# Kernel tuning notes

Measured on AMD Instinct MI355X. Metric: run time of the kernel, lower is better.

The kernel has to match this reference:

```python
import jax, jax.numpy as jnp
import numpy as np

N, D, H, E, TOP_K = 32768, 768, 256, 8, 2


def setup_inputs() -> dict:
    key = jax.random.key(0)
    ks = jax.random.split(key, 9)
    s_in = 1.0 / np.sqrt(D)
    s_hid = 1.0 / np.sqrt(H)
    return {
        "x": jax.random.normal(ks[0], (N, D), dtype=jnp.float32),
        # per-expert MLP weights, stacked over expert dim E
        "W1": jax.random.uniform(ks[1], (E, D, H), jnp.float32, -s_in, s_in),
        "b1": jax.random.uniform(ks[2], (E, H), jnp.float32, -s_in, s_in),
        "W2": jax.random.uniform(ks[3], (E, H, D), jnp.float32, -s_hid, s_hid),
        "b2": jax.random.uniform(ks[4], (E, D), jnp.float32, -s_hid, s_hid),
        # gate MLP: Linear(D,H) -> ReLU -> Linear(H,E)
        "Wg1": jax.random.uniform(ks[5], (D, H), jnp.float32, -s_in, s_in),
        "bg1": jax.random.uniform(ks[6], (H,), jnp.float32, -s_in, s_in),
        "Wg2": jax.random.uniform(ks[7], (H, E), jnp.float32, -s_hid, s_hid),
        "bg2": jax.random.uniform(ks[8], (E,), jnp.float32, -s_hid, s_hid),
    }


def reference(x, W1, b1, W2, b2, Wg1, bg1, Wg2, bg2):
    # gating
    gate_scores = jax.nn.relu(x @ Wg1 + bg1) @ Wg2 + bg2          # [N, E]
    gate_probs = jax.nn.softmax(gate_scores, axis=-1)              # [N, E]
    top_k_probs, top_k_idx = jax.lax.top_k(gate_probs, TOP_K)      # [N, K]
    top_k_probs = top_k_probs / jnp.sum(top_k_probs, axis=-1, keepdims=True)

    # dense all-expert compute (faithful to original: every expert on every token)
    h = jax.nn.relu(jnp.einsum("nd,edh->enh", x, W1) + b1[:, None, :])  # [E, N, H]
    expert_out = jnp.einsum("enh,ehd->end", h, W2) + b2[:, None, :]      # [E, N, D]

    # gather selected experts per token and combine
    tok = jnp.arange(x.shape[0])[:, None]                          # [N, 1]
    sel = expert_out[top_k_idx, tok, :]                            # [N, K, D]
    output = jnp.sum(top_k_probs[..., None] * sel, axis=1)          # [N, D]
    return output, gate_probs
```

## Files before the change

### kernel.cpp

```cpp
#include <hip/hip_runtime.h>
#include <hip/hip_bf16.h>
#include <stdint.h>

#define NTOK 32768
#define DIM  768
#define HID  256
#define NEXP 8
#define PADC 144

typedef float f32x4 __attribute__((ext_vector_type(4)));
typedef short s16x8 __attribute__((ext_vector_type(8)));

__device__ __forceinline__ unsigned short f2bf(float f) {
  union { float f; unsigned int u; } c; c.f = f;
  unsigned int r = c.u + 0x7fffu + ((c.u >> 16) & 1u);
  return (unsigned short)(r >> 16);
}

__device__ __forceinline__ float bf2f(unsigned int u) {
  union { unsigned int x; float f; } c; c.x = u << 16; return c.f;
}

__device__ __forceinline__ unsigned short f2h(float f) {
  union { _Float16 h; unsigned short u; } c; c.h = (_Float16)f; return c.u;
}

__device__ __forceinline__ float h2f(unsigned short u) {
  union { unsigned short u; _Float16 h; } c; c.u = u; return (float)c.h;
}

__device__ __forceinline__ void gload_lds16(const unsigned short* g, unsigned short* l) {
  __builtin_amdgcn_global_load_lds((const __attribute__((address_space(1))) void*)g,
                                   (__attribute__((address_space(3))) void*)l, 16, 0, 0);
}

__global__ __launch_bounds__(256) void k_cvt_x(const float* __restrict__ x,
                                               unsigned short* __restrict__ xf16) {
  int i = (blockIdx.x * 256 + threadIdx.x) * 8;
  float4 a = *(const float4*)(x + i);
  float4 b = *(const float4*)(x + i + 4);
  float f[8] = {a.x, a.y, a.z, a.w, b.x, b.y, b.z, b.w};
  unsigned short hh[8];
#pragma unroll
  for (int q = 0; q < 8; ++q) hh[q] = f2h(f[q]);
  int4 vh;
  vh.x = (int)((unsigned)hh[0] | ((unsigned)hh[1] << 16));
  vh.y = (int)((unsigned)hh[2] | ((unsigned)hh[3] << 16));
  vh.z = (int)((unsigned)hh[4] | ((unsigned)hh[5] << 16));
  vh.w = (int)((unsigned)hh[6] | ((unsigned)hh[7] << 16));
  *(int4*)(xf16 + i) = vh;
}

__global__ __launch_bounds__(256) void k_trall(const float* __restrict__ W1,
                                               const float* __restrict__ Wg1,
                                               const float* __restrict__ W2,
                                               unsigned short* __restrict__ w1t,
                                               unsigned short* __restrict__ wg1t,
                                               unsigned short* __restrict__ w2t) {
  __shared__ float tile[32][33];
  int z = blockIdx.z;
  const float* ip;
  unsigned short* op;
  int R, C;
  if (z < 8)       { ip = W1 + (size_t)z * DIM * HID;  op = w1t + (size_t)z * DIM * HID;  R = DIM; C = HID; }
  else if (z == 8) { ip = Wg1;                          op = wg1t;                          R = DIM; C = HID; }
  else             { ip = W2 + (size_t)(z - 9) * HID * DIM; op = w2t + (size_t)(z - 9) * HID * DIM; R = HID; C = DIM; }
  int r0 = blockIdx.y * 32, c0 = blockIdx.x * 32;
  if (r0 >= R || c0 >= C) return;
  int tx = threadIdx.x & 31, ty = threadIdx.x >> 5;
#pragma unroll
  for (int i = 0; i < 4; ++i)
    tile[ty + i * 8][tx] = ip[(size_t)(r0 + ty + i * 8) * C + c0 + tx];
  __syncthreads();
#pragma unroll
  for (int i = 0; i < 4; ++i)
    op[(size_t)(c0 + ty + i * 8) * R + r0 + tx] = f2h(tile[tx][ty + i * 8]);
}

__global__ __launch_bounds__(512) void k_gate1f(const unsigned short* __restrict__ xf16,
                                                const unsigned short* __restrict__ wg1t,
                                                const float* __restrict__ bg1,
                                                const float* __restrict__ wg2,
                                                const float* __restrict__ bg2,
                                                float* __restrict__ gs,
                                                int* __restrict__ rcnt,
                                                int* __restrict__ rlist) {
  int bm = blockIdx.x * 128;

  __shared__ __align__(16) unsigned short smem[(1024 + 2048) * 8];
  unsigned short* hs = smem;
  float* sc = (float*)&smem[16896];
  float* wg2s = (float*)&smem[20480];

  int tid = threadIdx.x;
  int lane = tid & 63;
  int wid = tid >> 6;
  int wm = wid >> 2, wn = wid & 3;
  int ar = lane & 15, kg = lane >> 4;

  const unsigned short* asrc[2];
  unsigned short* ldsA[2];
#pragma unroll
  for (int q = 0; q < 2; ++q) {
    int cb0 = q * 512 + wid * 64;
    int ci = cb0 + lane;
    int row = ci >> 3;
    int cb = (ci & 7) ^ (row & 7);
    asrc[q] = xf16 + (size_t)(bm + row) * DIM + cb * 8;
    ldsA[q] = &smem[cb0 * 8];
  }
  const unsigned short* bsrc[4];
  unsigned short* ldsB[4];
#pragma unroll
  for (int q = 0; q < 4; ++q) {
    int cb0 = q * 512 + wid * 64;
    int ci = cb0 + lane;
    int row = ci >> 3;
    int cb = (ci & 7) ^ (row & 7);
    bsrc[q] = wg1t + (size_t)row * DIM + cb * 8;
    ldsB[q] = &smem[8192 + cb0 * 8];
  }

  f32x4 acc[4][4] = {};

  for (int kt = 0; kt < DIM / 64; ++kt) {
#pragma unroll
    for (int q = 0; q < 2; ++q) gload_lds16(asrc[q] + kt * 64, ldsA[q]);
#pragma unroll
    for (int q = 0; q < 4; ++q) gload_lds16(bsrc[q] + kt * 64, ldsB[q]);
    __syncthreads();
#pragma unroll
    for (int ks = 0; ks < 2; ++ks) {
      int kc = ks * 4 + kg;
      s16x8 a[4], b[4];
#pragma unroll
      for (int m = 0; m < 4; ++m) {
        int row = wm * 64 + m * 16 + ar;
        a[m] = *(const s16x8*)&smem[row * 64 + ((kc ^ (row & 7)) * 8)];
      }
#pragma unroll
      for (int n = 0; n < 4; ++n) {
        int row = wn * 64 + n * 16 + ar;
        b[n] = *(const s16x8*)&smem[8192 + row * 64 + ((kc ^ (row & 7)) * 8)];
      }
#pragma unroll
      for (int m = 0; m < 4; ++m)
#pragma unroll
        for (int n = 0; n < 4; ++n)
          acc[m][n] = __builtin_amdgcn_mfma_f32_16x16x32_f16(a[m], b[n], acc[m][n], 0, 0, 0);
    }
    __syncthreads();
  }

#pragma unroll
  for (int j = 0; j < 4; ++j) wg2s[tid * 4 + j] = wg2[tid * 4 + j];

  int tok2 = (tid & 63) * 2;
  int ex = tid >> 6;
  float s0 = 0.f, s1 = 0.f;
#pragma unroll 1
  for (int half = 0; half < 2; ++half) {
    if ((wn >> 1) == half) {
#pragma unroll
      for (int n = 0; n < 4; ++n) {
        int col = (wn & 1) * 64 + n * 16 + ar;
        float bb = bg1[half * 128 + col];
#pragma unroll
        for (int m = 0; m < 4; ++m) {
          int rbase = wm * 64 + m * 16 + kg * 4;
#pragma unroll
          for (int r = 0; r < 4; ++r)
            hs[col * 132 + rbase + r] = f2h(fmaxf(acc[m][n][r] + bb, 0.f));
        }
      }
    }
    __syncthreads();
#pragma unroll 8
    for (int c = 0; c < 128; ++c) {
      unsigned int pair = *(const unsigned int*)&hs[c * 132 + tok2];
      float h0 = h2f((unsigned short)(pair & 0xffffu));
      float h1 = h2f((unsigned short)(pair >> 16));
      float w = wg2s[(half * 128 + c) * 8 + ex];
      s0 = fmaf(h0, w, s0);
      s1 = fmaf(h1, w, s1);
    }
    __syncthreads();
  }

  float b2e = bg2[ex];
  s0 += b2e; s1 += b2e;
  gs[(size_t)(bm + tok2) * 8 + ex] = s0;
  gs[(size_t)(bm + tok2 + 1) * 8 + ex] = s1;
  sc[tok2 * 8 + ex] = s0;
  sc[tok2 * 8 + 8 + ex] = s1;
  __syncthreads();

  if (tid < 128) {
    float m1 = -3e38f, m2 = -3e38f, m3 = -3e38f;
#pragma unroll
    for (int e = 0; e < 8; ++e) {
      float v = sc[tid * 8 + e];
      if (v > m1)      { m3 = m2; m2 = m1; m1 = v; }
      else if (v > m2) { m3 = m2; m2 = v; }
      else if (v > m3) { m3 = v; }
    }
    if (m2 - m3 < 1e-3f) {
      int i = atomicAdd(rcnt, 1);
      rlist[i] = bm + tid;
    }
  }
}

__global__ __launch_bounds__(256) void k_rescue(const float* __restrict__ x,
                                                const float* __restrict__ wg1,
                                                const float* __restrict__ bg1,
                                                const float* __restrict__ wg2,
                                                const float* __restrict__ bg2,
                                                const int* __restrict__ rcnt,
                                                const int* __restrict__ rlist,
                                                float* __restrict__ gs) {
  __shared__ float xs[DIM];
  __shared__ float ps[4][8];
  int n = rcnt[0];
  int tid = threadIdx.x;
  int lane = tid & 63, wid = tid >> 6;
  for (int idx = blockIdx.x; idx < n; idx += 2048) {
    int tok = rlist[idx];
    __syncthreads();
#pragma unroll
    for (int q = 0; q < 3; ++q) xs[tid + q * 256] = x[(size_t)tok * DIM + tid + q * 256];
    __syncthreads();
    const float* wcol = wg1 + tid;
    float pa[8] = {};
#pragma unroll 4
    for (int k0 = 0; k0 < DIM; k0 += 8) {
#pragma unroll
      for (int q = 0; q < 8; ++q)
        pa[q] = fmaf(xs[k0 + q], wcol[(size_t)(k0 + q) * HID], pa[q]);
    }
    float acc = bg1[tid] +
                (((pa[0] + pa[1]) + (pa[2] + pa[3])) + ((pa[4] + pa[5]) + (pa[6] + pa[7])));
    float hj = fmaxf(acc, 0.f);
    float p[8];
#pragma unroll
    for (int e = 0; e < 8; ++e) p[e] = hj * wg2[tid * 8 + e];
#pragma unroll
    for (int off = 32; off >= 1; off >>= 1) {
#pragma unroll
      for (int e = 0; e < 8; ++e) p[e] += __shfl_xor(p[e], off);
    }
    if (lane == 0) {
#pragma unroll
      for (int e = 0; e < 8; ++e) ps[wid][e] = p[e];
    }
    __syncthreads();
    if (tid < 8)
      gs[(size_t)tok * 8 + tid] = bg2[tid] + ps[0][tid] + ps[1][tid] + ps[2][tid] + ps[3][tid];
  }
}

__global__ __launch_bounds__(256) void k_gate2b(const float* __restrict__ gs,
                                                float* __restrict__ gprob,
                                                int* __restrict__ cnt,
                                                int* __restrict__ lists,
                                                float* __restrict__ wts) {
  __shared__ int lcnt[8];
  __shared__ int sbase[8];
  __shared__ int se1[256], se2[256], sp1[256], sp2[256];
  __shared__ float sw1[256], sw2[256];
  int tid = threadIdx.x;
  if (tid < 8) lcnt[tid] = 0;
  __syncthreads();

  int tok = blockIdx.x * 256 + tid;
  f32x4 s0v = *(const f32x4*)&gs[(size_t)tok * 8];
  f32x4 s1v = *(const f32x4*)&gs[(size_t)tok * 8 + 4];
  float s[8] = {s0v[0], s0v[1], s0v[2], s0v[3], s1v[0], s1v[1], s1v[2], s1v[3]};

  float m = s[0];
#pragma unroll
  for (int e = 1; e < 8; ++e) m = fmaxf(m, s[e]);
  float p[8]; float sum = 0.f;
#pragma unroll
  for (int e = 0; e < 8; ++e) { p[e] = expf(s[e] - m); sum += p[e]; }
  float inv = 1.f / sum;
#pragma unroll
  for (int e = 0; e < 8; ++e) p[e] *= inv;

  f32x4 o0 = {p[0], p[1], p[2], p[3]};
  f32x4 o1 = {p[4], p[5], p[6], p[7]};
  *(f32x4*)&gprob[(size_t)tok * 8] = o0;
  *(f32x4*)&gprob[(size_t)tok * 8 + 4] = o1;

  int e1 = 0; float p1 = p[0];
#pragma unroll
  for (int e = 1; e < 8; ++e) if (p[e] > p1) { p1 = p[e]; e1 = e; }
  int e2 = -1; float p2 = -1.f;
#pragma unroll
  for (int e = 0; e < 8; ++e) if (e != e1 && p[e] > p2) { p2 = p[e]; e2 = e; }
  float rinv = 1.f / (p1 + p2);

  int pos1 = atomicAdd(&lcnt[e1], 1);
  int pos2 = atomicAdd(&lcnt[e2], 1);
  se1[tid] = e1; sp1[tid] = pos1; sw1[tid] = p1 * rinv;
  se2[tid] = e2; sp2[tid] = pos2; sw2[tid] = p2 * rinv;
  __syncthreads();

  if (tid < 8) sbase[tid] = atomicAdd(&cnt[tid * 32], lcnt[tid]);
  __syncthreads();

  int a1i = sbase[se1[tid]] + sp1[tid];
  lists[se1[tid] * NTOK + a1i] = tok; wts[se1[tid] * NTOK + a1i] = sw1[tid];
  int a2i = sbase[se2[tid]] + sp2[tid];
  lists[se2[tid] * NTOK + a2i] = tok; wts[se2[tid] * NTOK + a2i] = -sw2[tid];
}

__global__ __launch_bounds__(512) void k_ffn1(const unsigned short* __restrict__ xf16,
                                              const unsigned short* __restrict__ w1t,
                                              const float* __restrict__ b1,
                                              const int* __restrict__ cnt,
                                              const int* __restrict__ lists,
                                              unsigned short* __restrict__ h) {
  int id = blockIdx.x;
  int xcd = id & 7, local = id >> 3;
  int xh = local & 31, e = local >> 5;
  int row0 = ((xh << 3) | xcd) * 128;

  int c = cnt[e * 32];
  if (row0 >= c) return;
  int pfx = 0;
#pragma unroll
  for (int j = 0; j < 8; ++j) if (j < e) pfx += cnt[j * 32];

  __shared__ __align__(16) unsigned short smem[(1024 + 2048) * 8];
  __shared__ int stok[128];

  int tid = threadIdx.x;
  int lane = tid & 63;
  int wid = tid >> 6;
  int wm = wid >> 2, wn = wid & 3;
  int ar = lane & 15, kg = lane >> 4;

  if (tid < 128) stok[tid] = lists[e * NTOK + min(row0 + tid, c - 1)];
  __syncthreads();

  const unsigned short* asrc[2];
  unsigned short* ldsA[2];
#pragma unroll
  for (int q = 0; q < 2; ++q) {
    int cb0 = q * 512 + wid * 64;
    int ci = cb0 + lane;
    int row = ci >> 3;
    int cb = (ci & 7) ^ (row & 7);
    asrc[q] = xf16 + (size_t)stok[row] * DIM + cb * 8;
    ldsA[q] = &smem[cb0 * 8];
  }
  const unsigned short* bsrc[4];
  unsigned short* ldsB[4];
#pragma unroll
  for (int q = 0; q < 4; ++q) {
    int cb0 = q * 512 + wid * 64;
    int ci = cb0 + lane;
    int row = ci >> 3;
    int cb = (ci & 7) ^ (row & 7);
    bsrc[q] = w1t + ((size_t)e * HID + row) * DIM + cb * 8;
    ldsB[q] = &smem[8192 + cb0 * 8];
  }

  f32x4 acc[4][4] = {};

  for (int kt = 0; kt < DIM / 64; ++kt) {
#pragma unroll
    for (int q = 0; q < 2; ++q) gload_lds16(asrc[q] + kt * 64, ldsA[q]);
#pragma unroll
    for (int q = 0; q < 4; ++q) gload_lds16(bsrc[q] + kt * 64, ldsB[q]);
    __syncthreads();
#pragma unroll
    for (int ks = 0; ks < 2; ++ks) {
      int kc = ks * 4 + kg;
      s16x8 a[4], b[4];
#pragma unroll
      for (int m = 0; m < 4; ++m) {
        int row = wm * 64 + m * 16 + ar;
        a[m] = *(const s16x8*)&smem[row * 64 + ((kc ^ (row & 7)) * 8)];
      }
#pragma unroll
      for (int n = 0; n < 4; ++n) {
        int row = wn * 64 + n * 16 + ar;
        b[n] = *(const s16x8*)&smem[8192 + row * 64 + ((kc ^ (row & 7)) * 8)];
      }
#pragma unroll
      for (int m = 0; m < 4; ++m)
#pragma unroll
        for (int n = 0; n < 4; ++n)
          acc[m][n] = __builtin_amdgcn_mfma_f32_16x16x32_f16(a[m], b[n], acc[m][n], 0, 0, 0);
    }
    __syncthreads();
  }

  int hbase = pfx + row0;
#pragma unroll 1
  for (int half = 0; half < 2; ++half) {
    if ((wn >> 1) == half) {
#pragma unroll
      for (int n = 0; n < 4; ++n) {
        int col = (wn & 1) * 64 + n * 16 + ar;
        float bb = b1[e * HID + half * 128 + col];
#pragma unroll
        for (int m = 0; m < 4; ++m) {
          int rloc = wm * 64 + m * 16 + kg * 4;
#pragma unroll
          for (int r = 0; r < 4; ++r)
            smem[(rloc + r) * PADC + col] = f2h(fmaxf(acc[m][n][r] + bb, 0.f));
        }
      }
    }
    __syncthreads();
#pragma unroll
    for (int q = 0; q < 4; ++q) {
      int ci = tid + q * 512;
      int row = ci >> 4, ch = ci & 15;
      if (row0 + row < c) {
        int4 v = *(const int4*)&smem[row * PADC + ch * 8];
        *(int4*)&h[(size_t)(hbase + row) * HID + half * 128 + ch * 8] = v;
      }
    }
    __syncthreads();
  }
}

template <bool STORE_PART>
__global__ __launch_bounds__(256) void k_ffn2(const unsigned short* __restrict__ h,
                                              const unsigned short* __restrict__ w2t,
                                              const float* __restrict__ b2,
                                              const int* __restrict__ cnt,
                                              const int* __restrict__ lists,
                                              const float* __restrict__ wts,
                                              unsigned short* __restrict__ part0,
                                              unsigned short* __restrict__ part1,
                                              float* __restrict__ out) {
  int id = blockIdx.x;
  int xcd = id & 7, local = id >> 3;
  int bny = local % 6;
  int r2 = local / 6;
  int xh = r2 & 31, e = r2 >> 5;
  int row0 = ((xh << 3) | xcd) * 128;
  int bn = bny * 128;

  int c = cnt[e * 32];
  if (row0 >= c) return;
  int pfx = 0;
#pragma unroll
  for (int j = 0; j < 8; ++j) if (j < e) pfx += cnt[j * 32];

  __shared__ __align__(16) unsigned short smem[128 * PADC];
  __shared__ int stok[128];
  __shared__ float swt[128];
  unsigned short* As = smem;
  unsigned short* Bs = smem + 128 * 64;

  int tid = threadIdx.x;
  int lane = tid & 63;
  int wid = tid >> 6;
  int wm = wid >> 1, wn = wid & 1;
  int ar = lane & 15, kg = lane >> 4;

  if (tid < 128) {
    int r = row0 + tid;
    stok[tid] = (r < c) ? lists[e * NTOK + r] : 0;
    swt[tid]  = (r < c) ? wts[e * NTOK + r] : 0.f;
  }
  __syncthreads();

  const unsigned short* asrc[4];
  const unsigned short* bsrc[4];
  unsigned short* ldsA[4];
  unsigned short* ldsB[4];
#pragma unroll
  for (int i = 0; i < 4; ++i) {
    int cb0 = i * 256 + wid * 64;
    int ci = cb0 + lane;
    int row = ci >> 3;
    int cb = (ci & 7) ^ (row & 7);
    asrc[i] = h + (size_t)(pfx + row0 + row) * HID + cb * 8;
    bsrc[i] = w2t + ((size_t)e * DIM + bn + row) * HID + cb * 8;
    ldsA[i] = &As[cb0 * 8];
    ldsB[i] = &Bs[cb0 * 8];
  }

  f32x4 acc[4][4] = {};

  for (int kt = 0; kt < HID / 64; ++kt) {
#pragma unroll
    for (int i = 0; i < 4; ++i) {
      gload_lds16(asrc[i] + kt * 64, ldsA[i]);
      gload_lds16(bsrc[i] + kt * 64, ldsB[i]);
    }
    __syncthreads();
#pragma unroll
    for (int ks = 0; ks < 2; ++ks) {
      int kc = ks * 4 + kg;
      s16x8 a[4], b[4];
#pragma unroll
      for (int m = 0; m < 4; ++m) {
        int row = wm * 64 + m * 16 + ar;
        a[m] = *(const s16x8*)&As[row * 64 + ((kc ^ (row & 7)) * 8)];
      }
#pragma unroll
      for (int n = 0; n < 4; ++n) {
        int row = wn * 64 + n * 16 + ar;
        b[n] = *(const s16x8*)&Bs[row * 64 + ((kc ^ (row & 7)) * 8)];
      }
#pragma unroll
      for (int m = 0; m < 4; ++m)
#pragma unroll
        for (int n = 0; n < 4; ++n)
          acc[m][n] = __builtin_amdgcn_mfma_f32_16x16x32_f16(a[m], b[n], acc[m][n], 0, 0, 0);
    }
    __syncthreads();
  }

  if constexpr (STORE_PART) {
#pragma unroll
    for (int n = 0; n < 4; ++n) {
      int col = wn * 64 + n * 16 + ar;
      float bb = b2[e * DIM + bn + col];
#pragma unroll
      for (int m = 0; m < 4; ++m) {
        int rloc = wm * 64 + m * 16 + kg * 4;
#pragma unroll
        for (int r = 0; r < 4; ++r) {
          float w = swt[rloc + r];
          smem[(rloc + r) * PADC + col] = f2bf((acc[m][n][r] + bb) * fabsf(w));
        }
      }
    }
    __syncthreads();
#pragma unroll
    for (int q = 0; q < 8; ++q) {
      int ci = tid + q * 256;
      int row = ci >> 4, ch = ci & 15;
      float w = swt[row];
      if (w != 0.f) {
        unsigned short* dst = (w > 0.f) ? part0 : part1;
        int4 v = *(const int4*)&smem[row * PADC + ch * 8];
        *(int4*)&dst[(size_t)stok[row] * DIM + bn + ch * 8] = v;
      }
    }
  } else {
#pragma unroll
    for (int n = 0; n < 4; ++n) {
      int col = bn + wn * 64 + n * 16 + ar;
      float bb = b2[e * DIM + col];
#pragma unroll
      for (int m = 0; m < 4; ++m) {
        int rloc = wm * 64 + m * 16 + kg * 4;
#pragma unroll
        for (int r = 0; r < 4; ++r) {
          float w = swt[rloc + r];
          if (w != 0.f) {
            float v = (acc[m][n][r] + bb) * fabsf(w);
            atomicAdd(&out[(size_t)stok[rloc + r] * DIM + col], v);
          }
        }
      }
    }
  }
}

__global__ __launch_bounds__(256) void k_combine(const unsigned short* __restrict__ p0,
                                                 const unsigned short* __restrict__ p1,
                                                 float* __restrict__ out) {
  size_t i = ((size_t)blockIdx.x * 256 + threadIdx.x) * 8;
  int4 a = *(const int4*)(p0 + i);
  int4 b = *(const int4*)(p1 + i);
  unsigned int ua[4] = {(unsigned)a.x, (unsigned)a.y, (unsigned)a.z, (unsigned)a.w};
  unsigned int ub[4] = {(unsigned)b.x, (unsigned)b.y, (unsigned)b.z, (unsigned)b.w};
  float o[8];
#pragma unroll
  for (int q = 0; q < 4; ++q) {
    o[q * 2 + 0] = bf2f(ua[q] & 0xffffu) + bf2f(ub[q] & 0xffffu);
    o[q * 2 + 1] = bf2f(ua[q] >> 16)     + bf2f(ub[q] >> 16);
  }
  *(float4*)(out + i)     = *(float4*)&o[0];
  *(float4*)(out + i + 4) = *(float4*)&o[4];
}

extern "C" void kernel_launch(void* const* d_in, const int* in_sizes, int n_in,
                              void* d_out, int out_size, void* d_ws, size_t ws_size,
                              hipStream_t stream) {
  const float* x   = (const float*)d_in[0];
  const float* W1  = (const float*)d_in[1];
  const float* b1  = (const float*)d_in[2];
  const float* W2  = (const float*)d_in[3];
  const float* b2  = (const float*)d_in[4];
  const float* Wg1 = (const float*)d_in[5];
  const float* bg1 = (const float*)d_in[6];
  const float* Wg2 = (const float*)d_in[7];
  const float* bg2 = (const float*)d_in[8];
  float* out = (float*)d_out;
  float* gprob = out + (size_t)NTOK * DIM;

  char* ws = (char*)d_ws;
  size_t off = 0;
  auto alloc = [&](size_t bytes) { void* pp = ws + off; off += (bytes + 255) & ~(size_t)255; return pp; };
  unsigned short* w1t = (unsigned short*)alloc((size_t)NEXP * HID * DIM * 2);
  unsigned short* w2t = (unsigned short*)alloc((size_t)NEXP * DIM * HID * 2);
  float* hgbuf = (float*)alloc((size_t)NTOK * HID * 4);
  int* cnt = (int*)alloc(NEXP * 32 * 4 + 256);
  int* lists = (int*)alloc((size_t)NEXP * NTOK * 4);
  float* wts = (float*)alloc((size_t)NEXP * NTOK * 4);
  unsigned short* part0 = (unsigned short*)alloc((size_t)NTOK * DIM * 2);
  unsigned short* part1 = (unsigned short*)alloc((size_t)NTOK * DIM * 2);
  bool store_mode = (off <= ws_size);

  int* rcnt = cnt + NEXP * 32;

  unsigned short *xf16, *wg1t;
  float* gs; int* rlist;
  if (store_mode) {
    xf16 = part1;
    wg1t = part0;
    char* p0b = (char*)part0;
    gs    = (float*)(p0b + (1u << 20));
    rlist = (int*)(p0b + 10 * (1u << 18));
  } else {
    xf16  = (unsigned short*)alloc((size_t)NTOK * DIM * 2);
    wg1t  = (unsigned short*)alloc((size_t)DIM * HID * 2);
    gs    = (float*)alloc((size_t)NTOK * 8 * 4);
    rlist = (int*)alloc((size_t)NTOK * 4);
  }

  unsigned short* h = (unsigned short*)hgbuf;

  hipMemsetAsync(cnt, 0, NEXP * 32 * sizeof(int) + 256, stream);
  if (!store_mode)
    hipMemsetAsync(d_out, 0, (size_t)NTOK * DIM * sizeof(float), stream);

  k_cvt_x<<<(NTOK * DIM) / (256 * 8), 256, 0, stream>>>(x, xf16);
  k_trall<<<dim3(DIM / 32, DIM / 32, 17), 256, 0, stream>>>(W1, Wg1, W2, w1t, wg1t, w2t);
  k_gate1f<<<NTOK / 128, 512, 0, stream>>>(xf16, wg1t, bg1, Wg2, bg2, gs, rcnt, rlist);
  k_rescue<<<2048, 256, 0, stream>>>(x, Wg1, bg1, Wg2, bg2, rcnt, rlist, gs);
  k_gate2b<<<NTOK / 256, 256, 0, stream>>>(gs, gprob, cnt, lists, wts);
  k_ffn1<<<(NTOK / 128) * NEXP, 512, 0, stream>>>(xf16, w1t, b1, cnt, lists, h);
  if (store_mode) {
    k_ffn2<true><<<(NTOK / 128) * 6 * NEXP, 256, 0, stream>>>(h, w2t, b2, cnt, lists, wts, part0, part1, out);
    k_combine<<<(NTOK * DIM) / (256 * 8), 256, 0, stream>>>(part0, part1, out);
  } else {
    k_ffn2<false><<<(NTOK / 128) * 6 * NEXP, 256, 0, stream>>>(h, w2t, b2, cnt, lists, wts, part0, part1, out);
  }
}
```

Baseline: 222.4 us.

## Store expert outputs contiguously in sorted order and gather them in combine

The second FFN kernel now writes each expert's output rows contiguously into a single sorted-order buffer instead of scattering them by token into two per-slot buffers. A per-token index records each token's (expert, position) pair, and the combine kernel gathers the two rows per token from it. The aim is to make the large FFN2 stores coalesced and sequential, at the cost of random-row reads in combine plus a small extra index buffer. The sign trick for choosing the slot is dropped and rows are bounds-checked by count instead.

```diff
diff --git a/kernel.cpp b/kernel.cpp
--- a/kernel.cpp
+++ b/kernel.cpp
@@ -263,7 +263,8 @@
                                                 float* __restrict__ gprob,
                                                 int* __restrict__ cnt,
                                                 int* __restrict__ lists,
-                                                float* __restrict__ wts) {
+                                                float* __restrict__ wts,
+                                                uint2* __restrict__ tokidx) {
   __shared__ int lcnt[8];
   __shared__ int sbase[8];
   __shared__ int se1[256], se2[256], sp1[256], sp2[256];
@@ -312,7 +313,9 @@
   int a1i = sbase[se1[tid]] + sp1[tid];
   lists[se1[tid] * NTOK + a1i] = tok; wts[se1[tid] * NTOK + a1i] = sw1[tid];
   int a2i = sbase[se2[tid]] + sp2[tid];
-  lists[se2[tid] * NTOK + a2i] = tok; wts[se2[tid] * NTOK + a2i] = -sw2[tid];
+  lists[se2[tid] * NTOK + a2i] = tok; wts[se2[tid] * NTOK + a2i] = sw2[tid];
+  tokidx[tok] = make_uint2(((unsigned)se1[tid] << 16) | (unsigned)a1i,
+                           ((unsigned)se2[tid] << 16) | (unsigned)a2i);
 }
 
 __global__ __launch_bounds__(512) void k_ffn1(const unsigned short* __restrict__ xf16,
@@ -436,8 +439,7 @@
                                               const int* __restrict__ cnt,
                                               const int* __restrict__ lists,
                                               const float* __restrict__ wts,
-                                              unsigned short* __restrict__ part0,
-                                              unsigned short* __restrict__ part1,
+                                              unsigned short* __restrict__ part,
                                               float* __restrict__ out) {
   int id = blockIdx.x;
   int xcd = id & 7, local = id >> 3;
@@ -531,20 +533,19 @@
 #pragma unroll
         for (int r = 0; r < 4; ++r) {
           float w = swt[rloc + r];
-          smem[(rloc + r) * PADC + col] = f2bf((acc[m][n][r] + bb) * fabsf(w));
+          smem[(rloc + r) * PADC + col] = f2bf((acc[m][n][r] + bb) * w);
         }
       }
     }
     __syncthreads();
+    int pbase = pfx + row0;
 #pragma unroll
     for (int q = 0; q < 8; ++q) {
       int ci = tid + q * 256;
       int row = ci >> 4, ch = ci & 15;
-      float w = swt[row];
-      if (w != 0.f) {
-        unsigned short* dst = (w > 0.f) ? part0 : part1;
+      if (row0 + row < c) {
         int4 v = *(const int4*)&smem[row * PADC + ch * 8];
-        *(int4*)&dst[(size_t)stok[row] * DIM + bn + ch * 8] = v;
+        *(int4*)&part[(size_t)(pbase + row) * DIM + bn + ch * 8] = v;
       }
     }
   } else {
@@ -557,9 +558,8 @@
         int rloc = wm * 64 + m * 16 + kg * 4;
 #pragma unroll
         for (int r = 0; r < 4; ++r) {
-          float w = swt[rloc + r];
-          if (w != 0.f) {
-            float v = (acc[m][n][r] + bb) * fabsf(w);
+          if (row0 + rloc + r < c) {
+            float v = (acc[m][n][r] + bb) * swt[rloc + r];
             atomicAdd(&out[(size_t)stok[rloc + r] * DIM + col], v);
           }
         }
@@ -568,22 +568,44 @@
   }
 }
 
-__global__ __launch_bounds__(256) void k_combine(const unsigned short* __restrict__ p0,
-                                                 const unsigned short* __restrict__ p1,
+__global__ __launch_bounds__(256) void k_combine(const unsigned short* __restrict__ part,
+                                                 const uint2* __restrict__ tokidx,
+                                                 const int* __restrict__ cnt,
                                                  float* __restrict__ out) {
-  size_t i = ((size_t)blockIdx.x * 256 + threadIdx.x) * 8;
-  int4 a = *(const int4*)(p0 + i);
-  int4 b = *(const int4*)(p1 + i);
-  unsigned int ua[4] = {(unsigned)a.x, (unsigned)a.y, (unsigned)a.z, (unsigned)a.w};
-  unsigned int ub[4] = {(unsigned)b.x, (unsigned)b.y, (unsigned)b.z, (unsigned)b.w};
-  float o[8];
-#pragma unroll
-  for (int q = 0; q < 4; ++q) {
-    o[q * 2 + 0] = bf2f(ua[q] & 0xffffu) + bf2f(ub[q] & 0xffffu);
-    o[q * 2 + 1] = bf2f(ua[q] >> 16)     + bf2f(ub[q] >> 16);
-  }
-  *(float4*)(out + i)     = *(float4*)&o[0];
-  *(float4*)(out + i + 4) = *(float4*)&o[4];
+  __shared__ int c1s[16], c2s[16];
+  int tid = threadIdx.x;
+  int t0 = blockIdx.x * 16;
+  if (tid < 16) {
+    uint2 ti = tokidx[t0 + tid];
+    int pfx[8];
+    int run = 0;
+#pragma unroll
+    for (int j = 0; j < 8; ++j) { pfx[j] = run; run += cnt[j * 32]; }
+    c1s[tid] = pfx[ti.x >> 16] + (int)(ti.x & 0xffffu);
+    c2s[tid] = pfx[ti.y >> 16] + (int)(ti.y & 0xffffu);
+  }
+  __syncthreads();
+  int row = tid >> 4;
+  int seg = tid & 15;
+  const unsigned short* p1 = part + (size_t)c1s[row] * DIM;
+  const unsigned short* p2 = part + (size_t)c2s[row] * DIM;
+  float* orow = out + (size_t)(t0 + row) * DIM;
+#pragma unroll
+  for (int j = 0; j < 6; ++j) {
+    int ch = seg * 6 + j;
+    int4 a = *(const int4*)(p1 + ch * 8);
+    int4 b = *(const int4*)(p2 + ch * 8);
+    unsigned int ua[4] = {(unsigned)a.x, (unsigned)a.y, (unsigned)a.z, (unsigned)a.w};
+    unsigned int ub[4] = {(unsigned)b.x, (unsigned)b.y, (unsigned)b.z, (unsigned)b.w};
+    float o[8];
+#pragma unroll
+    for (int q = 0; q < 4; ++q) {
+      o[q * 2 + 0] = bf2f(ua[q] & 0xffffu) + bf2f(ub[q] & 0xffffu);
+      o[q * 2 + 1] = bf2f(ua[q] >> 16)     + bf2f(ub[q] >> 16);
+    }
+    *(float4*)(orow + ch * 8)     = *(float4*)&o[0];
+    *(float4*)(orow + ch * 8 + 4) = *(float4*)&o[4];
+  }
 }
 
 extern "C" void kernel_launch(void* const* d_in, const int* in_sizes, int n_in,
@@ -610,8 +632,8 @@
   int* cnt = (int*)alloc(NEXP * 32 * 4 + 256);
   int* lists = (int*)alloc((size_t)NEXP * NTOK * 4);
   float* wts = (float*)alloc((size_t)NEXP * NTOK * 4);
-  unsigned short* part0 = (unsigned short*)alloc((size_t)NTOK * DIM * 2);
-  unsigned short* part1 = (unsigned short*)alloc((size_t)NTOK * DIM * 2);
+  uint2* tokidx = (uint2*)alloc((size_t)NTOK * 8);
+  unsigned short* part = (unsigned short*)alloc((size_t)2 * NTOK * DIM * 2);
   bool store_mode = (off <= ws_size);
 
   int* rcnt = cnt + NEXP * 32;
@@ -619,11 +641,11 @@
   unsigned short *xf16, *wg1t;
   float* gs; int* rlist;
   if (store_mode) {
-    xf16 = part1;
-    wg1t = part0;
-    char* p0b = (char*)part0;
-    gs    = (float*)(p0b + (1u << 20));
-    rlist = (int*)(p0b + 10 * (1u << 18));
+    char* pb = (char*)part;
+    wg1t  = (unsigned short*)pb;
+    gs    = (float*)(pb + (1u << 20));
+    rlist = (int*)(pb + 10 * (1u << 18));
+    xf16  = (unsigned short*)(pb + (4u << 20));
   } else {
     xf16  = (unsigned short*)alloc((size_t)NTOK * DIM * 2);
     wg1t  = (unsigned short*)alloc((size_t)DIM * HID * 2);
@@ -641,12 +663,12 @@
   k_trall<<<dim3(DIM / 32, DIM / 32, 17), 256, 0, stream>>>(W1, Wg1, W2, w1t, wg1t, w2t);
   k_gate1f<<<NTOK / 128, 512, 0, stream>>>(xf16, wg1t, bg1, Wg2, bg2, gs, rcnt, rlist);
   k_rescue<<<2048, 256, 0, stream>>>(x, Wg1, bg1, Wg2, bg2, rcnt, rlist, gs);
-  k_gate2b<<<NTOK / 256, 256, 0, stream>>>(gs, gprob, cnt, lists, wts);
+  k_gate2b<<<NTOK / 256, 256, 0, stream>>>(gs, gprob, cnt, lists, wts, tokidx);
   k_ffn1<<<(NTOK / 128) * NEXP, 512, 0, stream>>>(xf16, w1t, b1, cnt, lists, h);
   if (store_mode) {
-    k_ffn2<true><<<(NTOK / 128) * 6 * NEXP, 256, 0, stream>>>(h, w2t, b2, cnt, lists, wts, part0, part1, out);
-    k_combine<<<(NTOK * DIM) / (256 * 8), 256, 0, stream>>>(part0, part1, out);
+    k_ffn2<true><<<(NTOK / 128) * 6 * NEXP, 256, 0, stream>>>(h, w2t, b2, cnt, lists, wts, part, out);
+    k_combine<<<NTOK / 16, 256, 0, stream>>>(part, tokidx, cnt, out);
   } else {
-    k_ffn2<false><<<(NTOK / 128) * 6 * NEXP, 256, 0, stream>>>(h, w2t, b2, cnt, lists, wts, part0, part1, out);
-  }
-}
+    k_ffn2<false><<<(NTOK / 128) * 6 * NEXP, 256, 0, stream>>>(h, w2t, b2, cnt, lists, wts, part, out);
+  }
+}
```

After: 237.7 us. 1.07x slower.
